# Kernel tuning notes

Measured on AMD Instinct MI355X. Metric: run time of the kernel, lower is better.

The kernel has to match this reference:

```python
import jax, jax.numpy as jnp
import numpy as np

# Two-link planar arm parameters (match init_kwargs)
L1, L2 = 1.0, 1.0      # link lengths
C1, C2 = 0.5, 0.5      # COM distances
M1, M2 = 1.0, 1.0      # masses
I1, I2 = 0.1, 0.1      # link inertias
G = 9.81

B = 8388608


def setup_inputs() -> dict:
    key = jax.random.key(0)
    k1, k2, k3 = jax.random.split(key, 3)
    q = jax.random.normal(k1, (B, 2), dtype=jnp.float32)
    dq = jax.random.normal(k2, (B, 2), dtype=jnp.float32)
    tau = jax.random.normal(k3, (B, 2), dtype=jnp.float32)
    return {"q": q, "dq": dq, "tau": tau}


def _qdd(q, dq, tau):
    # q, dq, tau: [B, 2]
    q1, q2 = q[..., 0], q[..., 1]
    dq1, dq2 = dq[..., 0], dq[..., 1]
    c2 = jnp.cos(q2)
    s2 = jnp.sin(q2)

    # Inertia matrix M(q), symmetric positive definite
    alpha = I1 + M1 * C1 * C1 + I2 + M2 * (L1 * L1 + C2 * C2)
    beta = M2 * L1 * C2
    delta = I2 + M2 * C2 * C2
    M11 = alpha + 2.0 * beta * c2
    M12 = delta + beta * c2
    M22 = jnp.full_like(M11, delta)

    # Coriolis/centrifugal + gravity h(q, dq)
    g1 = (M1 * C1 + M2 * L1) * G * jnp.cos(q1) + M2 * C2 * G * jnp.cos(q1 + q2)
    g2 = M2 * C2 * G * jnp.cos(q1 + q2)
    h1 = -beta * s2 * (2.0 * dq1 * dq2 + dq2 * dq2) + g1
    h2 = beta * s2 * dq1 * dq1 + g2

    r1 = tau[..., 0] - h1
    r2 = tau[..., 1] - h2

    # Closed-form 2x2 solve (M symmetric: M21 == M12)
    det = M11 * M22 - M12 * M12
    qdd1 = (M22 * r1 - M12 * r2) / det
    qdd2 = (M11 * r2 - M12 * r1) / det
    return jnp.stack([qdd1, qdd2], axis=-1)


def reference(q, dq, tau):
    return _qdd(q, dq, tau)
```

## Files before the change

### kernel.cpp

```cpp
#include <hip/hip_runtime.h>
#include <cstdint>


__global__ __launch_bounds__(256) void fd_qdd_kernel(
    const float4* __restrict__ qp,
    const float4* __restrict__ dqp,
    const float4* __restrict__ taup,
    float4* __restrict__ outp,
    int nvec)
{
    int i = blockIdx.x * blockDim.x + threadIdx.x;
    if (i >= nvec) return;

    float4 qv = qp[i];
    float4 dv = dqp[i];
    float4 tv = taup[i];
    float4 ov;

    const float alpha = 1.7f;
    const float beta  = 0.5f;
    const float delta = 0.35f;
    const float G     = 9.81f;
    const float gA    = 1.5f * G;
    const float gB    = 0.5f * G;

    const float* qs = (const float*)&qv;
    const float* ds = (const float*)&dv;
    const float* ts = (const float*)&tv;
    float*       os = (float*)&ov;

#pragma unroll
    for (int j = 0; j < 2; ++j) {
        float q1   = qs[2 * j + 0];
        float q2   = qs[2 * j + 1];
        float dq1  = ds[2 * j + 0];
        float dq2  = ds[2 * j + 1];
        float tau1 = ts[2 * j + 0];
        float tau2 = ts[2 * j + 1];

        float c2 = __cosf(q2);
        float s2 = __sinf(q2);

        float M11 = alpha + 2.0f * beta * c2;
        float M12 = delta + beta * c2;
        float M22 = delta;

        float cq1  = __cosf(q1);
        float cq12 = __cosf(q1 + q2);

        float g1 = gA * cq1 + gB * cq12;
        float g2 = gB * cq12;

        float h1 = -beta * s2 * (2.0f * dq1 * dq2 + dq2 * dq2) + g1;
        float h2 =  beta * s2 * dq1 * dq1 + g2;

        float r1 = tau1 - h1;
        float r2 = tau2 - h2;

        float det  = M11 * M22 - M12 * M12;
        float rdet = __frcp_rn(det);

        float qdd1 = (M22 * r1 - M12 * r2) * rdet;
        float qdd2 = (M11 * r2 - M12 * r1) * rdet;

        os[2 * j + 0] = qdd1;
        os[2 * j + 1] = qdd2;
    }

    outp[i] = ov;
}

extern "C" void kernel_launch(void* const* d_in, const int* in_sizes, int n_in,
                              void* d_out, int out_size, void* d_ws, size_t ws_size,
                              hipStream_t stream) {
    const float4* q   = (const float4*)d_in[0];
    const float4* dq  = (const float4*)d_in[1];
    const float4* tau = (const float4*)d_in[2];
    float4*       out = (float4*)d_out;

    int n_elems = in_sizes[0];
    int nvec    = n_elems / 4;

    int block = 256;
    int grid  = (nvec + block - 1) / block;
    fd_qdd_kernel<<<grid, block, 0, stream>>>(q, dq, tau, out, nvec);
}
```

Baseline: 211.2 us.

## Use grid-stride loop with two-way unroll and nontemporal output stores

Replaces the one-thread-per-vector launch with a fixed 2048x256 grid-stride loop that processes two float4 groups per iteration, so more loads are in flight per thread. Output is written with nontemporal stores to reduce cache pollution. The correctly rounded reciprocal is swapped for the hardware approximate rcp. The kernel is memory-bound streaming, so gains depend on whether the persistent grid keeps enough bytes in flight. The approximate reciprocal adds a small accuracy risk.

```diff
diff --git a/kernel.cpp b/kernel.cpp
--- a/kernel.cpp
+++ b/kernel.cpp
@@ -2,21 +2,12 @@
 #include <cstdint>
 
 
-__global__ __launch_bounds__(256) void fd_qdd_kernel(
-    const float4* __restrict__ qp,
-    const float4* __restrict__ dqp,
-    const float4* __restrict__ taup,
-    float4* __restrict__ outp,
-    int nvec)
-{
-    int i = blockIdx.x * blockDim.x + threadIdx.x;
-    if (i >= nvec) return;
+#define BLOCK 256
+#define GRID  2048
 
-    float4 qv = qp[i];
-    float4 dv = dqp[i];
-    float4 tv = taup[i];
-    float4 ov;
+typedef float f4 __attribute__((ext_vector_type(4)));
 
+__device__ __forceinline__ f4 fd_compute(f4 qv, f4 dv, f4 tv) {
     const float alpha = 1.7f;
     const float beta  = 0.5f;
     const float delta = 0.35f;
@@ -24,19 +15,16 @@
     const float gA    = 1.5f * G;
     const float gB    = 0.5f * G;
 
-    const float* qs = (const float*)&qv;
-    const float* ds = (const float*)&dv;
-    const float* ts = (const float*)&tv;
-    float*       os = (float*)&ov;
+    f4 ov;
 
 #pragma unroll
     for (int j = 0; j < 2; ++j) {
-        float q1   = qs[2 * j + 0];
-        float q2   = qs[2 * j + 1];
-        float dq1  = ds[2 * j + 0];
-        float dq2  = ds[2 * j + 1];
-        float tau1 = ts[2 * j + 0];
-        float tau2 = ts[2 * j + 1];
+        float q1   = qv[2 * j + 0];
+        float q2   = qv[2 * j + 1];
+        float dq1  = dv[2 * j + 0];
+        float dq2  = dv[2 * j + 1];
+        float tau1 = tv[2 * j + 0];
+        float tau2 = tv[2 * j + 1];
 
         float c2 = __cosf(q2);
         float s2 = __sinf(q2);
@@ -58,30 +46,57 @@
         float r2 = tau2 - h2;
 
         float det  = M11 * M22 - M12 * M12;
-        float rdet = __frcp_rn(det);
+        float rdet = __builtin_amdgcn_rcpf(det);
 
-        float qdd1 = (M22 * r1 - M12 * r2) * rdet;
-        float qdd2 = (M11 * r2 - M12 * r1) * rdet;
+        ov[2 * j + 0] = (M22 * r1 - M12 * r2) * rdet;
+        ov[2 * j + 1] = (M11 * r2 - M12 * r1) * rdet;
+    }
+    return ov;
+}
 
-        os[2 * j + 0] = qdd1;
-        os[2 * j + 1] = qdd2;
+__global__ __launch_bounds__(BLOCK) void fd_qdd_kernel(
+    const f4* __restrict__ qp,
+    const f4* __restrict__ dqp,
+    const f4* __restrict__ taup,
+    f4* __restrict__ outp,
+    int nvec)
+{
+    const int tid = blockIdx.x * BLOCK + threadIdx.x;
+    const int nt  = GRID * BLOCK;
+    const int nt2 = 2 * nt;
+
+    int idx = tid;
+    for (; idx + nt < nvec; idx += nt2) {
+        int i0 = idx, i1 = idx + nt;
+        f4 q0 = qp[i0];
+        f4 d0 = dqp[i0];
+        f4 t0 = taup[i0];
+        f4 q1 = qp[i1];
+        f4 d1 = dqp[i1];
+        f4 t1 = taup[i1];
+
+        f4 o0 = fd_compute(q0, d0, t0);
+        f4 o1 = fd_compute(q1, d1, t1);
+
+        __builtin_nontemporal_store(o0, &outp[i0]);
+        __builtin_nontemporal_store(o1, &outp[i1]);
     }
-
-    outp[i] = ov;
+    if (idx < nvec) {
+        f4 o = fd_compute(qp[idx], dqp[idx], taup[idx]);
+        __builtin_nontemporal_store(o, &outp[idx]);
+    }
 }
 
 extern "C" void kernel_launch(void* const* d_in, const int* in_sizes, int n_in,
                               void* d_out, int out_size, void* d_ws, size_t ws_size,
                               hipStream_t stream) {
-    const float4* q   = (const float4*)d_in[0];
-    const float4* dq  = (const float4*)d_in[1];
-    const float4* tau = (const float4*)d_in[2];
-    float4*       out = (float4*)d_out;
+    const f4* q   = (const f4*)d_in[0];
+    const f4* dq  = (const f4*)d_in[1];
+    const f4* tau = (const f4*)d_in[2];
+    f4*       out = (f4*)d_out;
 
     int n_elems = in_sizes[0];
     int nvec    = n_elems / 4;
 
-    int block = 256;
-    int grid  = (nvec + block - 1) / block;
-    fd_qdd_kernel<<<grid, block, 0, stream>>>(q, dq, tau, out, nvec);
+    fd_qdd_kernel<<<GRID, BLOCK, 0, stream>>>(q, dq, tau, out, nvec);
 }
```

Measured after the change: 217.5 us. +3.0%, slower.
